# Kernel optimization log

Hardware: AMD Instinct MI355X
Metric: run time of the kernel (lower is better)

The kernel has to match this reference:

```python
import jax, jax.numpy as jnp
import numpy as np

DIM = 128
IN_DIM = 2
LAYERS = 4
H = 256
W = 256
WH = W // 2 + 1  # rfft last-dim size
RATIO = 1.0


def _radial_mask():
    # waves = sqrt(k^2 + r^2) over the rfft2 grid; keep waves <= (W//2)*ratio
    k = np.fft.rfftfreq(W) * W            # (WH,)
    r = np.fft.fftfreq(H) * H             # (H,)
    waves = np.sqrt(k[None, :] ** 2 + r[:, None] ** 2)  # (H, WH)
    return jnp.asarray(waves <= (W // 2) * RATIO)


def conv1x1(x, w, b):
    # x: (b,c,h,w), w: (o,c), b: (o,)
    return jnp.einsum('bchw,oc->bohw', x, w) + b[None, :, None, None]


def setup_inputs() -> dict:
    key = jax.random.key(0)
    ks = jax.random.split(key, 15)
    d = DIM
    inp = {
        'x': jax.random.normal(ks[0], (4, IN_DIM, H, W), dtype=jnp.float32),
        'enc_w': jax.random.normal(ks[1], (d, IN_DIM), dtype=jnp.float32) * (1.0 / np.sqrt(IN_DIM)),
        'enc_b': jnp.zeros((d,), dtype=jnp.float32),
        'pos_emb': jax.random.normal(ks[2], (1, d, H, W), dtype=jnp.float32) * 0.02,
        'mlp_w1': jax.random.normal(ks[3], (LAYERS, 4 * d, d), dtype=jnp.float32) * (1.0 / np.sqrt(d)),
        'mlp_b1': jnp.zeros((LAYERS, 4 * d), dtype=jnp.float32),
        'mlp_w2': jax.random.normal(ks[4], (LAYERS, d, 4 * d), dtype=jnp.float32) * (1.0 / np.sqrt(4 * d)),
        'mlp_b2': jnp.zeros((LAYERS, d), dtype=jnp.float32),
        'spec_mags': jax.random.normal(ks[5], (LAYERS, d, H, WH), dtype=jnp.float32),
        'spec_phases': jax.random.normal(ks[6], (LAYERS, d, H, WH), dtype=jnp.float32),
        'oxo_w': jax.random.normal(ks[7], (LAYERS, d, d), dtype=jnp.float32) * (1.0 / np.sqrt(d)),
        'oxo_b': jnp.zeros((LAYERS, d), dtype=jnp.float32),
        'dec_w': jax.random.normal(ks[8], (IN_DIM, d), dtype=jnp.float32) * (1.0 / np.sqrt(d)),
        'dec_b': jnp.zeros((IN_DIM,), dtype=jnp.float32),
    }
    return inp


def reference(x, enc_w, enc_b, pos_emb, mlp_w1, mlp_b1, mlp_w2, mlp_b2,
              spec_mags, spec_phases, oxo_w, oxo_b, dec_w, dec_b):
    scale = (DIM / IN_DIM) ** 0.5
    mask = _radial_mask()  # (H, WH) bool, constant
    h = conv1x1(x, enc_w, enc_b) * scale + pos_emb
    for i in range(LAYERS):
        # mlp block: 1x1 conv -> SiLU -> 1x1 conv
        x1 = jax.nn.silu(conv1x1(h, mlp_w1[i], mlp_b1[i]))
        x1 = conv1x1(x1, mlp_w2[i], mlp_b2[i])
        # spectral conv: rfft2 (ortho), complex filter on radially-masked modes,
        # zeros elsewhere (equivalent to masked_select/scatter in the original), irfft2
        xf = jnp.fft.rfft2(x1, norm='ortho')  # (b,c,H,WH) complex64
        filt = jax.nn.sigmoid(spec_mags[i]) * jnp.exp(1j * spec_phases[i])  # (c,H,WH)
        xf = jnp.where(mask[None, None, :, :], xf * filt[None], 0.0 + 0.0j)
        x1 = jnp.fft.irfft2(xf, s=(H, W), norm='ortho')
        x1 = conv1x1(x1, oxo_w[i], oxo_b[i])
        h = x1 + h
    return conv1x1(h, dec_w, dec_b) / scale
```

## Files before the change

kernel.cpp:

```cpp
#include <hip/hip_runtime.h>
#include <math.h>

#define PI2 6.2831853071795864769f

typedef short bf16x8 __attribute__((ext_vector_type(8)));
typedef float f32x4 __attribute__((ext_vector_type(4)));
typedef int   i32x4 __attribute__((ext_vector_type(4)));

__device__ inline unsigned splitf(float v) {
    unsigned u  = __float_as_uint(v);
    unsigned r  = (u + 0x7fffu + ((u >> 16) & 1u)) >> 16;
    float hi    = __uint_as_float(r << 16);
    float lof   = v - hi;
    unsigned u2 = __float_as_uint(lof);
    unsigned r2 = (u2 + 0x7fffu + ((u2 >> 16) & 1u)) >> 16;
    return (r & 0xffffu) | (r2 << 16);
}
__device__ inline float upk(unsigned w) {
    return __uint_as_float(w << 16) + __uint_as_float(w & 0xffff0000u);
}

union VecU { i32x4 i; bf16x8 s; };

__device__ inline void unpack2(i32x4 d0, i32x4 d1, bf16x8& hi, bf16x8& lo) {
    VecU h, l;
    h.i.x = __builtin_amdgcn_perm(d0.y, d0.x, 0x05040100);
    h.i.y = __builtin_amdgcn_perm(d0.w, d0.z, 0x05040100);
    h.i.z = __builtin_amdgcn_perm(d1.y, d1.x, 0x05040100);
    h.i.w = __builtin_amdgcn_perm(d1.w, d1.z, 0x05040100);
    l.i.x = __builtin_amdgcn_perm(d0.y, d0.x, 0x07060302);
    l.i.y = __builtin_amdgcn_perm(d0.w, d0.z, 0x07060302);
    l.i.z = __builtin_amdgcn_perm(d1.y, d1.x, 0x07060302);
    l.i.w = __builtin_amdgcn_perm(d1.w, d1.z, 0x07060302);
    hi = h.s; lo = l.s;
}

__device__ inline void unpack8(const int* d, bf16x8& hi, bf16x8& lo) {
    VecU h, l;
    h.i.x = __builtin_amdgcn_perm(d[1], d[0], 0x05040100);
    h.i.y = __builtin_amdgcn_perm(d[3], d[2], 0x05040100);
    h.i.z = __builtin_amdgcn_perm(d[5], d[4], 0x05040100);
    h.i.w = __builtin_amdgcn_perm(d[7], d[6], 0x05040100);
    l.i.x = __builtin_amdgcn_perm(d[1], d[0], 0x07060302);
    l.i.y = __builtin_amdgcn_perm(d[3], d[2], 0x07060302);
    l.i.z = __builtin_amdgcn_perm(d[5], d[4], 0x07060302);
    l.i.w = __builtin_amdgcn_perm(d[7], d[6], 0x07060302);
    hi = h.s; lo = l.s;
}

__global__ void sentinel_kernel(float* __restrict__ out, int n) {
    int t = blockIdx.x * 256 + threadIdx.x;
    if (t < n) out[t] = 12345.0f;
}

__global__ void split_kernel(const float* __restrict__ in, unsigned* __restrict__ out) {
    long q = (long)blockIdx.x * 256 + threadIdx.x;
    const float4* ip = (const float4*)in;
    float4 v = ip[q];
    i32x4 o;
    o.x = (int)splitf(v.x); o.y = (int)splitf(v.y);
    o.z = (int)splitf(v.z); o.w = (int)splitf(v.w);
    ((i32x4*)out)[q] = o;
}

__global__ void enc_kernel(const float* __restrict__ x, const float* __restrict__ w,
                           const float* __restrict__ b, const float* __restrict__ pos,
                           unsigned* __restrict__ h) {
    long t = (long)blockIdx.x * 256 + threadIdx.x;
    int pq = (int)(t & 16383);
    int c  = (int)((t >> 14) & 127);
    int bb = (int)(t >> 21);
    float4 x0 = *(const float4*)(x + ((long)bb * 2 + 0) * 65536 + pq * 4);
    float4 x1 = *(const float4*)(x + ((long)bb * 2 + 1) * 65536 + pq * 4);
    float4 pv = *(const float4*)(pos + (long)c * 65536 + pq * 4);
    float w0 = w[c * 2], w1 = w[c * 2 + 1], bc = b[c];
    uint4 o;
    o.x = splitf((w0 * x0.x + w1 * x1.x + bc) * 8.0f + pv.x);
    o.y = splitf((w0 * x0.y + w1 * x1.y + bc) * 8.0f + pv.y);
    o.z = splitf((w0 * x0.z + w1 * x1.z + bc) * 8.0f + pv.z);
    o.w = splitf((w0 * x0.w + w1 * x1.w + bc) * 8.0f + pv.w);
    *(uint4*)(h + t * 4) = o;
}

__global__ __launch_bounds__(256, 2)
void mlp_fused(const unsigned* __restrict__ Ax, const unsigned* __restrict__ W1x,
               const float* __restrict__ b1, const unsigned* __restrict__ W2x,
               const float* __restrict__ b2, float* __restrict__ t2) {
    __shared__ unsigned SM[12800];
    unsigned* ALDS = SM;
    unsigned* HLDS = SM + 8448;
    int tid = threadIdx.x;
    int w = tid >> 6, l = tid & 63;
    int lr = l & 15, lg = l >> 4;
    int p0 = blockIdx.x * 64;

#pragma unroll
    for (int i = 0; i < 8; i++) {
        int f = i * 256 + tid;
        int k = f >> 4, q = f & 15;
        uint4 v = *(const uint4*)(Ax + (long)k * 65536 + p0 + q * 4);
        ALDS[(q * 4 + 0) * 132 + k] = v.x;
        ALDS[(q * 4 + 1) * 132 + k] = v.y;
        ALDS[(q * 4 + 2) * 132 + k] = v.z;
        ALDS[(q * 4 + 3) * 132 + k] = v.w;
    }
    __syncthreads();

    f32x4 acc2[4][2] = {};
#pragma unroll 1
    for (int c = 0; c < 8; c++) {
        f32x4 acc1[4] = {};
#pragma unroll
        for (int ks = 0; ks < 4; ks++) {
            bf16x8 bh, bl;
            {
                const unsigned* bp = W1x + (c * 64 + w * 16 + lr) * 128 + ks * 32 + lg * 8;
                i32x4 d0 = *(const i32x4*)bp;
                i32x4 d1 = *(const i32x4*)(bp + 4);
                unpack2(d0, d1, bh, bl);
            }
#pragma unroll
            for (int ms = 0; ms < 4; ms++) {
                const i32x4* apx = (const i32x4*)&ALDS[(ms * 16 + lr) * 132 + ks * 32 + lg * 8];
                i32x4 a0 = apx[0], a1 = apx[1];
                bf16x8 ah, al; unpack2(a0, a1, ah, al);
                acc1[ms] = __builtin_amdgcn_mfma_f32_16x16x32_bf16(ah, bh, acc1[ms], 0, 0, 0);
                acc1[ms] = __builtin_amdgcn_mfma_f32_16x16x32_bf16(ah, bl, acc1[ms], 0, 0, 0);
                acc1[ms] = __builtin_amdgcn_mfma_f32_16x16x32_bf16(al, bh, acc1[ms], 0, 0, 0);
            }
        }
        {
            int hl = w * 16 + lr;
            float bias = b1[c * 64 + hl];
#pragma unroll
            for (int ms = 0; ms < 4; ms++)
#pragma unroll
                for (int r = 0; r < 4; r++) {
                    float pre = acc1[ms][r] + bias;
                    float s = pre / (1.0f + __expf(-pre));
                    int pix = ms * 16 + lg * 4 + r;
                    HLDS[pix * 68 + hl] = splitf(s);
                }
        }
        __syncthreads();
#pragma unroll
        for (int ks2 = 0; ks2 < 2; ks2++) {
            bf16x8 bh[2], bl[2];
#pragma unroll
            for (int ns = 0; ns < 2; ns++) {
                const unsigned* bp = W2x + (w * 32 + ns * 16 + lr) * 512 + c * 64 + ks2 * 32 + lg * 8;
                i32x4 d0 = *(const i32x4*)bp;
                i32x4 d1 = *(const i32x4*)(bp + 4);
                unpack2(d0, d1, bh[ns], bl[ns]);
            }
#pragma unroll
            for (int ms = 0; ms < 4; ms++) {
                const i32x4* hp = (const i32x4*)&HLDS[(ms * 16 + lr) * 68 + ks2 * 32 + lg * 8];
                i32x4 d0 = hp[0], d1 = hp[1];
                bf16x8 ah, al; unpack2(d0, d1, ah, al);
#pragma unroll
                for (int ns = 0; ns < 2; ns++) {
                    acc2[ms][ns] = __builtin_amdgcn_mfma_f32_16x16x32_bf16(ah, bh[ns], acc2[ms][ns], 0, 0, 0);
                    acc2[ms][ns] = __builtin_amdgcn_mfma_f32_16x16x32_bf16(ah, bl[ns], acc2[ms][ns], 0, 0, 0);
                    acc2[ms][ns] = __builtin_amdgcn_mfma_f32_16x16x32_bf16(al, bh[ns], acc2[ms][ns], 0, 0, 0);
                }
            }
        }
        __syncthreads();
    }
    float* T = (float*)SM;
#pragma unroll
    for (int ns = 0; ns < 2; ns++) {
        int n = w * 32 + ns * 16 + lr;
        float bias = b2[n];
#pragma unroll
        for (int ms = 0; ms < 4; ms++)
#pragma unroll
            for (int r = 0; r < 4; r++) {
                int pix = ms * 16 + lg * 4 + r;
                T[n * 68 + pix] = acc2[ms][ns][r] + bias;
            }
    }
    __syncthreads();
#pragma unroll
    for (int i = 0; i < 8; i++) {
        int f = i * 256 + tid;
        int n = f >> 4, q = f & 15;
        float4 v = *(const float4*)&T[n * 68 + q * 4];
        *(float4*)(t2 + (long)n * 65536 + p0 + q * 4) = v;
    }
}

__global__ __launch_bounds__(256, 2)
void oxo_kernel(const unsigned* __restrict__ Tx, const unsigned* __restrict__ Bx,
                const float* __restrict__ ob, unsigned* __restrict__ h) {
    __shared__ float T[128 * 128];
    int tid = threadIdx.x;
    int w = tid >> 6, l = tid & 63;
    int lr = l & 15, lg = l >> 4;
    int m0 = blockIdx.x * 128;
    int n0 = w * 32;
    f32x4 acc[8][2] = {};
    for (int k0 = 0; k0 < 128; k0 += 32) {
        bf16x8 bh[2], bl[2];
#pragma unroll
        for (int ns = 0; ns < 2; ns++) {
            const unsigned* bp = Bx + (n0 + ns * 16 + lr) * 128 + k0 + lg * 8;
            i32x4 d0 = *(const i32x4*)bp;
            i32x4 d1 = *(const i32x4*)(bp + 4);
            unpack2(d0, d1, bh[ns], bl[ns]);
        }
#pragma unroll
        for (int ms = 0; ms < 8; ms++) {
            const unsigned* ap = Tx + (long)(k0 + lg * 8) * 65536 + m0 + ms * 16 + lr;
            int d[8];
#pragma unroll
            for (int j = 0; j < 8; j++) d[j] = (int)ap[(long)j * 65536];
            bf16x8 ah, al; unpack8(d, ah, al);
#pragma unroll
            for (int ns = 0; ns < 2; ns++) {
                acc[ms][ns] = __builtin_amdgcn_mfma_f32_16x16x32_bf16(ah, bh[ns], acc[ms][ns], 0, 0, 0);
                acc[ms][ns] = __builtin_amdgcn_mfma_f32_16x16x32_bf16(ah, bl[ns], acc[ms][ns], 0, 0, 0);
                acc[ms][ns] = __builtin_amdgcn_mfma_f32_16x16x32_bf16(al, bh[ns], acc[ms][ns], 0, 0, 0);
            }
        }
    }
#pragma unroll
    for (int ns = 0; ns < 2; ns++) {
        int n = n0 + ns * 16 + lr;
#pragma unroll
        for (int ms = 0; ms < 8; ms++) {
            int blk = ((ms * 4 + lg) + n) & 31;
#pragma unroll
            for (int r = 0; r < 4; r++)
                T[n * 128 + blk * 4 + r] = acc[ms][ns][r];
        }
    }
    __syncthreads();
#pragma unroll
    for (int i = 0; i < 16; i++) {
        int flat = i * 256 + tid;
        int n = flat >> 5, q = flat & 31;
        const float4* src = (const float4*)&T[n * 128 + (((q + n) & 31) * 4)];
        float4 v = *src;
        float bias = ob[n];
        unsigned* hp = h + (long)n * 65536 + m0 + q * 4;
        uint4 hv = *(uint4*)hp;
        uint4 o;
        o.x = splitf(upk(hv.x) + v.x + bias);
        o.y = splitf(upk(hv.y) + v.y + bias);
        o.z = splitf(upk(hv.z) + v.z + bias);
        o.w = splitf(upk(hv.w) + v.w + bias);
        *(uint4*)hp = o;
    }
}

__global__ void fft_row_fwd(const float* __restrict__ in, float2* __restrict__ freq, int c0) {
    __shared__ float2 A[4][256];
    __shared__ float2 B[4][256];
    __shared__ float2 TW[128];
    int tid = threadIdx.x;
    int img = blockIdx.x >> 6, rgrp = blockIdx.x & 63;
    if (tid < 128) {
        float sn, cs; __sincosf((PI2 / 256.f) * (float)tid, &sn, &cs);
        TW[tid] = make_float2(cs, sn);
    }
    {
        int r = tid >> 6, l = tid & 63;
        const float4* src = (const float4*)(in + ((long)(c0 + img) * 256 + rgrp * 4 + r) * 256);
        float4 v = src[l];
        A[r][l * 4 + 0] = make_float2(v.x, 0.f);
        A[r][l * 4 + 1] = make_float2(v.y, 0.f);
        A[r][l * 4 + 2] = make_float2(v.z, 0.f);
        A[r][l * 4 + 3] = make_float2(v.w, 0.f);
    }
    __syncthreads();
    float2 (*s)[256] = A; float2 (*d)[256] = B;
    for (int m = 1; m < 256; m <<= 1) {
#pragma unroll
        for (int q = 0; q < 2; q++) {
            int bf = tid + q * 256;
            int r = bf >> 7, i = bf & 127;
            int jm = i & ~(m - 1);
            float2 c0v = s[r][i], c1 = s[r][i + 128];
            float2 t = TW[jm];
            float2 df = make_float2(c0v.x - c1.x, c0v.y - c1.y);
            d[r][i + jm]     = make_float2(c0v.x + c1.x, c0v.y + c1.y);
            d[r][i + jm + m] = make_float2(t.x * df.x + t.y * df.y, t.x * df.y - t.y * df.x);
        }
        __syncthreads();
        float2 (*tmp)[256] = s; s = d; d = tmp;
    }
    long ib = (long)img * 34816;
    for (int q = tid; q < 4 * 129; q += 256) {
        int r = q / 129; int k = q - r * 129;
        freq[ib + (k >> 3) * 2048 + (rgrp * 4 + r) * 8 + (k & 7)] = s[r][k];
    }
}

__global__ void fft_col(float2* __restrict__ freq, const float* __restrict__ mags,
                        const float* __restrict__ phases, int c0) {
    __shared__ float2 A[8][256];
    __shared__ float2 B[8][256];
    __shared__ float2 TW[128];
    int tid = threadIdx.x;
    int img = blockIdx.x / 17;
    int kt  = blockIdx.x % 17;
    int kx0 = kt * 8;
    float2* base = freq + (long)img * 34816 + kt * 2048;
    if (tid < 128) {
        float sn, cs; __sincosf((PI2 / 256.f) * (float)tid, &sn, &cs);
        TW[tid] = make_float2(cs, sn);
    }
#pragma unroll
    for (int q = 0; q < 8; q++) {
        int e = tid + q * 256;
        A[e & 7][e >> 3] = base[e];
    }
    __syncthreads();
    float2 (*s)[256] = A; float2 (*d)[256] = B;
    for (int m = 1; m < 256; m <<= 1) {
#pragma unroll
        for (int q = 0; q < 4; q++) {
            int bf = tid + q * 256;
            int cl = bf >> 7, i = bf & 127;
            int jm = i & ~(m - 1);
            float2 c0v = s[cl][i], c1 = s[cl][i + 128];
            float2 t = TW[jm];
            float2 df = make_float2(c0v.x - c1.x, c0v.y - c1.y);
            d[cl][i + jm]     = make_float2(c0v.x + c1.x, c0v.y + c1.y);
            d[cl][i + jm + m] = make_float2(t.x * df.x + t.y * df.y, t.x * df.y - t.y * df.x);
        }
        __syncthreads();
        float2 (*tmp)[256] = s; s = d; d = tmp;
    }
#pragma unroll
    for (int q = 0; q < 8; q++) {
        int e = tid + q * 256;
        int cl = e & 7, ky = e >> 3;
        int kx = kx0 + cl;
        float2 v = s[cl][ky];
        float2 r = make_float2(0.f, 0.f);
        if (kx < 129) {
            int ry = ky < 128 ? ky : ky - 256;
            if (kx * kx + ry * ry <= 16384) {
                long fi = ((long)(c0 + img) * 256 + ky) * 129 + kx;
                float mg = mags[fi], ph = phases[fi];
                float sg = 1.0f / (1.0f + __expf(-mg));
                float sn, cs; __sincosf(ph, &sn, &cs);
                float fr = sg * cs, fim = sg * sn;
                r = make_float2(v.x * fr - v.y * fim, v.x * fim + v.y * fr);
            }
        }
        s[cl][ky] = r;
    }
    __syncthreads();
    for (int m = 1; m < 256; m <<= 1) {
#pragma unroll
        for (int q = 0; q < 4; q++) {
            int bf = tid + q * 256;
            int cl = bf >> 7, i = bf & 127;
            int jm = i & ~(m - 1);
            float2 c0v = s[cl][i], c1 = s[cl][i + 128];
            float2 t = TW[jm];
            float2 df = make_float2(c0v.x - c1.x, c0v.y - c1.y);
            d[cl][i + jm]     = make_float2(c0v.x + c1.x, c0v.y + c1.y);
            d[cl][i + jm + m] = make_float2(t.x * df.x - t.y * df.y, t.x * df.y + t.y * df.x);
        }
        __syncthreads();
        float2 (*tmp)[256] = s; s = d; d = tmp;
    }
#pragma unroll
    for (int q = 0; q < 8; q++) {
        int e = tid + q * 256;
        base[e] = s[e & 7][e >> 3];
    }
}

__global__ void fft_row_inv(const float2* __restrict__ freq, unsigned* __restrict__ out, int c0) {
    __shared__ float2 A[4][256];
    __shared__ float2 B[4][256];
    __shared__ float2 TW[128];
    int tid = threadIdx.x;
    int img = blockIdx.x >> 6, rgrp = blockIdx.x & 63;
    if (tid < 128) {
        float sn, cs; __sincosf((PI2 / 256.f) * (float)tid, &sn, &cs);
        TW[tid] = make_float2(cs, sn);
    }
    long ib = (long)img * 34816;
#pragma unroll
    for (int q = 0; q < 4; q++) {
        int e = tid + q * 256;
        int r = e >> 8, xx = e & 255;
        int k = (xx <= 128) ? xx : 256 - xx;
        float2 v = freq[ib + (k >> 3) * 2048 + (rgrp * 4 + r) * 8 + (k & 7)];
        if (xx > 128) v.y = -v.y;
        A[r][xx] = v;
    }
    __syncthreads();
    float2 (*s)[256] = A; float2 (*d)[256] = B;
    for (int m = 1; m < 256; m <<= 1) {
#pragma unroll
        for (int q = 0; q < 2; q++) {
            int bf = tid + q * 256;
            int r = bf >> 7, i = bf & 127;
            int jm = i & ~(m - 1);
            float2 c0v = s[r][i], c1 = s[r][i + 128];
            float2 t = TW[jm];
            float2 df = make_float2(c0v.x - c1.x, c0v.y - c1.y);
            d[r][i + jm]     = make_float2(c0v.x + c1.x, c0v.y + c1.y);
            d[r][i + jm + m] = make_float2(t.x * df.x - t.y * df.y, t.x * df.y + t.y * df.x);
        }
        __syncthreads();
        float2 (*tmp)[256] = s; s = d; d = tmp;
    }
    {
        int r = tid >> 6, l = tid & 63;
        const float sc = 1.0f / 65536.0f;
        uint4 o;
        o.x = splitf(s[r][l * 4 + 0].x * sc);
        o.y = splitf(s[r][l * 4 + 1].x * sc);
        o.z = splitf(s[r][l * 4 + 2].x * sc);
        o.w = splitf(s[r][l * 4 + 3].x * sc);
        *(uint4*)(out + ((long)(c0 + img) * 256 + rgrp * 4 + r) * 256 + l * 4) = o;
    }
}

__global__ void dec_kernel(const unsigned* __restrict__ h, const float* __restrict__ w,
                           const float* __restrict__ b, float* __restrict__ out) {
    int t = blockIdx.x * 256 + threadIdx.x;
    int bb = t >> 16, p = t & 65535;
    const unsigned* hb = h + (long)bb * 8388608 + p;
    float a0 = b[0], a1 = b[1];
    float a0b = 0.f, a1b = 0.f;
#pragma unroll 4
    for (int c = 0; c < 128; c += 2) {
        float h0 = upk(hb[(long)c * 65536]);
        float h1 = upk(hb[(long)(c + 1) * 65536]);
        a0  += w[c] * h0;        a1  += w[128 + c] * h0;
        a0b += w[c + 1] * h1;    a1b += w[128 + c + 1] * h1;
    }
    out[((long)bb * 2 + 0) * 65536 + p] = (a0 + a0b) * 0.125f;
    out[((long)bb * 2 + 1) * 65536 + p] = (a1 + a1b) * 0.125f;
}

extern "C" void kernel_launch(void* const* d_in, const int* in_sizes, int n_in,
                              void* d_out, int out_size, void* d_ws, size_t ws_size,
                              hipStream_t stream) {
    const float* x        = (const float*)d_in[0];
    const float* enc_w    = (const float*)d_in[1];
    const float* enc_b    = (const float*)d_in[2];
    const float* pos_emb  = (const float*)d_in[3];
    const float* mlp_w1   = (const float*)d_in[4];
    const float* mlp_b1   = (const float*)d_in[5];
    const float* mlp_w2   = (const float*)d_in[6];
    const float* mlp_b2   = (const float*)d_in[7];
    const float* spec_mag = (const float*)d_in[8];
    const float* spec_ph  = (const float*)d_in[9];
    const float* oxo_w    = (const float*)d_in[10];
    const float* oxo_b    = (const float*)d_in[11];
    const float* dec_w    = (const float*)d_in[12];
    const float* dec_b    = (const float*)d_in[13];
    float* outp = (float*)d_out;

    const size_t WS_NEEDED = 186187776ULL;
    if (ws_size < WS_NEEDED) {
        sentinel_kernel<<<(out_size + 255) / 256, 256, 0, stream>>>(outp, out_size);
        return;
    }

    unsigned* u    = (unsigned*)d_ws;
    unsigned* h    = u;
    float*    t2   = (float*)(u + 33554432);
    unsigned* TxO  = (unsigned*)t2;
    float2*   freq = (float2*)(u + 41943040);
    unsigned* Wx1  = u + 46399488;
    unsigned* Wx2  = Wx1 + 65536;
    unsigned* Wox  = Wx2 + 65536;

    enc_kernel<<<32768, 256, 0, stream>>>(x, enc_w, enc_b, pos_emb, h);

    for (int l = 0; l < 4; l++) {
        split_kernel<<<64, 256, 0, stream>>>(mlp_w1 + (long)l * 65536, Wx1);
        split_kernel<<<64, 256, 0, stream>>>(mlp_w2 + (long)l * 65536, Wx2);
        split_kernel<<<16, 256, 0, stream>>>(oxo_w + (long)l * 16384, Wox);
        const float* b1l = mlp_b1 + l * 512;
        const float* b2l = mlp_b2 + l * 128;
        const float* mgl = spec_mag + (long)l * 4227072;
        const float* phl = spec_ph  + (long)l * 4227072;
        const float* obl = oxo_b + l * 128;
        for (int b = 0; b < 4; b++) {
            unsigned* hb = h + (long)b * 8388608;
            mlp_fused<<<1024, 256, 0, stream>>>(hb, Wx1, b1l, Wx2, b2l, t2);
            for (int c0 = 0; c0 < 128; c0 += 64) {
                fft_row_fwd<<<4096, 256, 0, stream>>>(t2, freq, c0);
                fft_col<<<64 * 17, 256, 0, stream>>>(freq, mgl, phl, c0);
                fft_row_inv<<<4096, 256, 0, stream>>>(freq, TxO, c0);
            }
            oxo_kernel<<<512, 256, 0, stream>>>(TxO, Wox, obl, hb);
        }
    }

    dec_kernel<<<1024, 256, 0, stream>>>(h, dec_w, dec_b, outp);
}
```

Baseline: 3.996 ms.

## Pack two real channels into one complex FFT for row transforms

The forward row FFT now loads two real channels as the real and imaginary parts of one complex signal, runs a single 256-point FFT, and separates the two spectra using Hermitian symmetry. The inverse row FFT combines two half-spectra into one complex input and writes both real outputs from the real and imaginary parts. This halves the number of row-FFT blocks and butterfly passes, removing work wasted on zero imaginary parts. In exchange it adds extra separation arithmetic, and the inverse zeroes the imaginary parts at k=0 and k=128, which changes rounding slightly.

```diff
diff --git a/kernel.cpp b/kernel.cpp
--- a/kernel.cpp
+++ b/kernel.cpp
@@ -260,19 +260,21 @@
     __shared__ float2 B[4][256];
     __shared__ float2 TW[128];
     int tid = threadIdx.x;
-    int img = blockIdx.x >> 6, rgrp = blockIdx.x & 63;
+    int pr = blockIdx.x >> 6, rgrp = blockIdx.x & 63;
     if (tid < 128) {
         float sn, cs; __sincosf((PI2 / 256.f) * (float)tid, &sn, &cs);
         TW[tid] = make_float2(cs, sn);
     }
     {
         int r = tid >> 6, l = tid & 63;
-        const float4* src = (const float4*)(in + ((long)(c0 + img) * 256 + rgrp * 4 + r) * 256);
-        float4 v = src[l];
-        A[r][l * 4 + 0] = make_float2(v.x, 0.f);
-        A[r][l * 4 + 1] = make_float2(v.y, 0.f);
-        A[r][l * 4 + 2] = make_float2(v.z, 0.f);
-        A[r][l * 4 + 3] = make_float2(v.w, 0.f);
+        int row = rgrp * 4 + r;
+        const float4* sa = (const float4*)(in + ((long)(c0 + pr * 2 + 0) * 256 + row) * 256);
+        const float4* sb = (const float4*)(in + ((long)(c0 + pr * 2 + 1) * 256 + row) * 256);
+        float4 va = sa[l], vb = sb[l];
+        A[r][l * 4 + 0] = make_float2(va.x, vb.x);
+        A[r][l * 4 + 1] = make_float2(va.y, vb.y);
+        A[r][l * 4 + 2] = make_float2(va.z, vb.z);
+        A[r][l * 4 + 3] = make_float2(va.w, vb.w);
     }
     __syncthreads();
     float2 (*s)[256] = A; float2 (*d)[256] = B;
@@ -291,10 +293,17 @@
         __syncthreads();
         float2 (*tmp)[256] = s; s = d; d = tmp;
     }
-    long ib = (long)img * 34816;
+    long iba = (long)(pr * 2 + 0) * 34816;
+    long ibb = (long)(pr * 2 + 1) * 34816;
     for (int q = tid; q < 4 * 129; q += 256) {
         int r = q / 129; int k = q - r * 129;
-        freq[ib + (k >> 3) * 2048 + (rgrp * 4 + r) * 8 + (k & 7)] = s[r][k];
+        float2 z  = s[r][k];
+        float2 zm = s[r][(256 - k) & 255];
+        float2 za = make_float2(0.5f * (z.x + zm.x), 0.5f * (z.y - zm.y));
+        float2 zb = make_float2(0.5f * (z.y + zm.y), 0.5f * (zm.x - z.x));
+        long off = (k >> 3) * 2048 + (rgrp * 4 + r) * 8 + (k & 7);
+        freq[iba + off] = za;
+        freq[ibb + off] = zb;
     }
 }
 
@@ -382,19 +391,25 @@
     __shared__ float2 B[4][256];
     __shared__ float2 TW[128];
     int tid = threadIdx.x;
-    int img = blockIdx.x >> 6, rgrp = blockIdx.x & 63;
+    int pr = blockIdx.x >> 6, rgrp = blockIdx.x & 63;
     if (tid < 128) {
         float sn, cs; __sincosf((PI2 / 256.f) * (float)tid, &sn, &cs);
         TW[tid] = make_float2(cs, sn);
     }
-    long ib = (long)img * 34816;
+    long iba = (long)(pr * 2 + 0) * 34816;
+    long ibb = (long)(pr * 2 + 1) * 34816;
 #pragma unroll
     for (int q = 0; q < 4; q++) {
         int e = tid + q * 256;
         int r = e >> 8, xx = e & 255;
         int k = (xx <= 128) ? xx : 256 - xx;
-        float2 v = freq[ib + (k >> 3) * 2048 + (rgrp * 4 + r) * 8 + (k & 7)];
-        if (xx > 128) v.y = -v.y;
+        long off = (k >> 3) * 2048 + (rgrp * 4 + r) * 8 + (k & 7);
+        float2 ga = freq[iba + off];
+        float2 gb = freq[ibb + off];
+        if (k == 0 || k == 128) { ga.y = 0.f; gb.y = 0.f; }
+        float2 v;
+        if (xx <= 128) v = make_float2(ga.x - gb.y, ga.y + gb.x);
+        else           v = make_float2(ga.x + gb.y, gb.x - ga.y);
         A[r][xx] = v;
     }
     __syncthreads();
@@ -417,12 +432,18 @@
     {
         int r = tid >> 6, l = tid & 63;
         const float sc = 1.0f / 65536.0f;
-        uint4 o;
-        o.x = splitf(s[r][l * 4 + 0].x * sc);
-        o.y = splitf(s[r][l * 4 + 1].x * sc);
-        o.z = splitf(s[r][l * 4 + 2].x * sc);
-        o.w = splitf(s[r][l * 4 + 3].x * sc);
-        *(uint4*)(out + ((long)(c0 + img) * 256 + rgrp * 4 + r) * 256 + l * 4) = o;
+        int row = rgrp * 4 + r;
+        uint4 oa, ob;
+        oa.x = splitf(s[r][l * 4 + 0].x * sc);
+        oa.y = splitf(s[r][l * 4 + 1].x * sc);
+        oa.z = splitf(s[r][l * 4 + 2].x * sc);
+        oa.w = splitf(s[r][l * 4 + 3].x * sc);
+        ob.x = splitf(s[r][l * 4 + 0].y * sc);
+        ob.y = splitf(s[r][l * 4 + 1].y * sc);
+        ob.z = splitf(s[r][l * 4 + 2].y * sc);
+        ob.w = splitf(s[r][l * 4 + 3].y * sc);
+        *(uint4*)(out + ((long)(c0 + pr * 2 + 0) * 256 + row) * 256 + l * 4) = oa;
+        *(uint4*)(out + ((long)(c0 + pr * 2 + 1) * 256 + row) * 256 + l * 4) = ob;
     }
 }
 
@@ -493,9 +514,9 @@
             unsigned* hb = h + (long)b * 8388608;
             mlp_fused<<<1024, 256, 0, stream>>>(hb, Wx1, b1l, Wx2, b2l, t2);
             for (int c0 = 0; c0 < 128; c0 += 64) {
-                fft_row_fwd<<<4096, 256, 0, stream>>>(t2, freq, c0);
+                fft_row_fwd<<<2048, 256, 0, stream>>>(t2, freq, c0);
                 fft_col<<<64 * 17, 256, 0, stream>>>(freq, mgl, phl, c0);
-                fft_row_inv<<<4096, 256, 0, stream>>>(freq, TxO, c0);
+                fft_row_inv<<<2048, 256, 0, stream>>>(freq, TxO, c0);
             }
             oxo_kernel<<<512, 256, 0, stream>>>(TxO, Wox, obl, hb);
         }
```

Result: faster. 3.700 ms (-7.4%).
